# Kernel tuning notes

Hardware: AMD Instinct MI355X
Metric: run time of the kernel (lower is better)

Reference implementation:

```python
import jax, jax.numpy as jnp
import numpy as np

HEADS, DQK, DV = 4, 128, 128
HH, WW = 32, 32
SCALE = DQK ** -0.5
EPS = 1e-5


def bn(x, g, b, m, v):
    # eval-mode BatchNorm2d over channel dim of NCHW
    inv = g * jax.lax.rsqrt(v + EPS)
    return x * inv[:, None, None] + (b - m * inv)[:, None, None]


def rel_to_abs(x):
    # x: (B, Nh, L, 2L-1) -> (B, Nh, L, L)
    B, Nh, L, _ = x.shape
    x = jnp.pad(x, ((0, 0), (0, 0), (0, 0), (0, 1)))
    fx = x.reshape(B, Nh, L * 2 * L)
    fx = jnp.pad(fx, ((0, 0), (0, 0), (0, L - 1)))
    fx = fx.reshape(B, Nh, L + 1, 2 * L - 1)
    return fx[:, :, :L, L - 1:]


def rel_logits_1d(q, rel_k):
    # q: (B, Nh, H, W, D); rel_k: (2W-1, D)
    B, Nh, H, W, D = q.shape
    r = jnp.einsum('bnhwd,rd->bnhwr', q, rel_k)
    r = rel_to_abs(r.reshape(B, Nh * H, W, 2 * W - 1))
    r = r.reshape(B, Nh, H, W, W)
    return jnp.broadcast_to(r[:, :, :, None], (B, Nh, H, H, W, W))


def pos_bias(q, rel_h, rel_w):
    # q: (B, Nh, H*W, D), already scaled
    B, Nh, L, D = q.shape
    q5 = q.reshape(B, Nh, HH, WW, D)
    rw = rel_logits_1d(q5, rel_w)                     # (B,N,H,Hx,W,W)
    rw = rw.transpose(0, 1, 2, 4, 3, 5).reshape(B, Nh, HH * WW, HH * WW)
    rh = rel_logits_1d(q5.transpose(0, 1, 3, 2, 4), rel_h)  # (B,N,W,Wx,H,H)
    rh = rh.transpose(0, 1, 4, 2, 5, 3).reshape(B, Nh, HH * WW, HH * WW)
    return rw + rh


def to_heads(x):
    # (B, Nh*d, H, W) -> (B, Nh, H*W, d)
    B, C, H, W = x.shape
    x = x.reshape(B, HEADS, C // HEADS, H, W)
    return x.transpose(0, 1, 3, 4, 2).reshape(B, HEADS, H * W, C // HEADS)


def mhsa(x, w_qk, w_v, rel_h, rel_w):
    B, C, H, W = x.shape
    qk = jnp.einsum('bchw,oc->bohw', x, w_qk)
    q, k = jnp.split(qk, 2, axis=1)
    v = jnp.einsum('bchw,oc->bohw', x, w_v)
    q, k, v = to_heads(q), to_heads(k), to_heads(v)
    q = q * SCALE
    logits = jnp.einsum('bnid,bnjd->bnij', q, k) + pos_bias(q, rel_h, rel_w)
    weights = jax.nn.softmax(logits, axis=-1)
    out = jnp.einsum('bnij,bnjd->bnid', weights, v)   # (B,Nh,HW,dv)
    out = out.reshape(B, HEADS, H, W, DV).transpose(0, 1, 4, 2, 3)
    return out.reshape(B, HEADS * DV, H, W)


def setup_inputs() -> dict:
    key = jax.random.key(0)
    ks = jax.random.split(key, 12)
    d = {
        'x': jax.random.normal(ks[0], (8, 512, HH, WW), jnp.float32),
        'w_qk': jax.random.normal(ks[1], (2 * HEADS * DQK, 512), jnp.float32) * 0.02,
        'w_v': jax.random.normal(ks[2], (HEADS * DV, 512), jnp.float32) * 0.02,
        'rel_h': jax.random.normal(ks[3], (2 * HH - 1, DQK), jnp.float32) * SCALE,
        'rel_w': jax.random.normal(ks[4], (2 * WW - 1, DQK), jnp.float32) * SCALE,
        'g1': jnp.ones((512,), jnp.float32),
        'b1': jnp.zeros((512,), jnp.float32),
        'm1': jax.random.normal(ks[5], (512,), jnp.float32) * 0.1,
        'v1': jax.random.uniform(ks[6], (512,), jnp.float32) + 0.5,
        'g2': jnp.ones((512,), jnp.float32),
        'b2': jnp.zeros((512,), jnp.float32),
        'm2': jax.random.normal(ks[7], (512,), jnp.float32) * 0.1,
        'v2': jax.random.uniform(ks[8], (512,), jnp.float32) + 0.5,
        'w_fc': jax.random.normal(ks[9], (512, 512, 3, 3), jnp.float32) * 0.02,
        'bias_fc': jnp.zeros((512,), jnp.float32),
    }
    return d


def reference(x, w_qk, w_v, rel_h, rel_w, g1, b1, m1, v1, g2, b2, m2, v2, w_fc, bias_fc):
    out = jax.nn.relu(bn(x, g1, b1, m1, v1))
    out = mhsa(out, w_qk, w_v, rel_h, rel_w)
    x = out + x
    out = jax.nn.relu(bn(x, g2, b2, m2, v2))
    out = jax.lax.conv_general_dilated(
        out, w_fc, window_strides=(1, 1), padding='SAME',
        dimension_numbers=('NCHW', 'OIHW', 'NCHW')) + bias_fc[:, None, None]
    return out + x
```

## Files before the change

kernel.cpp:

```cpp
#include <hip/hip_runtime.h>

typedef __bf16 v8bf __attribute__((ext_vector_type(8)));
typedef float f32x4 __attribute__((ext_vector_type(4)));

#define DEVI static __device__ __forceinline__

DEVI v8bf load8(const __bf16* p) { return *reinterpret_cast<const v8bf*>(p); }

DEVI f32x4 mfma16(v8bf a, v8bf b, f32x4 c) {
  return __builtin_amdgcn_mfma_f32_16x16x32_bf16(a, b, c, 0, 0, 0);
}

DEVI void gld16(const __bf16* g, __bf16* l) {
  __builtin_amdgcn_global_load_lds(
      (const __attribute__((address_space(1))) unsigned int*)(const void*)g,
      (__attribute__((address_space(3))) unsigned int*)(void*)l, 16, 0, 0);
}

#define SCALE_Q 0.08838834764831845f

__global__ void k_prep(const float* __restrict__ wqk, const float* __restrict__ wv,
                       const float* __restrict__ relh, const float* __restrict__ relw,
                       const float* __restrict__ wfc, __bf16* __restrict__ wqkb,
                       __bf16* __restrict__ wvb, __bf16* __restrict__ rhb,
                       __bf16* __restrict__ rwb, __bf16* __restrict__ Wt,
                       float* __restrict__ zpad4) {
  const int bid = blockIdx.x, tid = threadIdx.x;
  if (bid < 2048) {
    int i = bid * 256 + tid;
    wqkb[i] = (__bf16)wqk[i];
  } else if (bid < 3072) {
    int i = (bid - 2048) * 256 + tid;
    wvb[i] = (__bf16)wv[i];
  } else if (bid < 3104) {
    int i = (bid - 3072) * 256 + tid;
    if (i < 8064) rhb[i] = (__bf16)relh[i];
  } else if (bid < 3136) {
    int i = (bid - 3104) * 256 + tid;
    if (i < 8064) rwb[i] = (__bf16)relw[i];
  } else if (bid < 4160) {
    int i = (bid - 3136) * 256 + tid;
    const float* src = wfc + (size_t)i * 9;
#pragma unroll
    for (int tap = 0; tap < 9; ++tap)
      Wt[(size_t)tap * 262144 + i] = (__bf16)src[tap];
  } else {
    int i = (bid - 4160) * 256 + tid;
    f32x4 z = {0.f, 0.f, 0.f, 0.f};
    reinterpret_cast<f32x4*>(zpad4)[i] = z;
  }
}

__global__ void k_bn1(const float* __restrict__ x, const float* __restrict__ g,
                      const float* __restrict__ bb, const float* __restrict__ m,
                      const float* __restrict__ v, __bf16* __restrict__ y) {
  __shared__ float tile[32][33];
  const int b = blockIdx.z, c0 = blockIdx.y * 32, s0 = blockIdx.x * 32;
  const int tx = threadIdx.x, ty = threadIdx.y;
#pragma unroll
  for (int r = 0; r < 4; ++r) {
    int c = c0 + ty + r * 8;
    float inv = g[c] * rsqrtf(v[c] + 1e-5f);
    float beta = bb[c] - m[c] * inv;
    float val = x[((size_t)b * 512 + c) * 1024 + s0 + tx] * inv + beta;
    tile[ty + r * 8][tx] = fmaxf(val, 0.0f);
  }
  __syncthreads();
#pragma unroll
  for (int r = 0; r < 4; ++r) {
    int s = s0 + ty + r * 8;
    y[((size_t)b * 1024 + s) * 512 + c0 + tx] = (__bf16)tile[tx][ty + r * 8];
  }
}

__global__ void k_bn2c(float* o0x2, const float* __restrict__ o1,
                       const float* __restrict__ lp, const float* __restrict__ xin,
                       const float* __restrict__ g, const float* __restrict__ bb,
                       const float* __restrict__ m, const float* __restrict__ v,
                       __bf16* __restrict__ zp) {
  __shared__ float tile[32][33];
  const int b = blockIdx.z, c0 = blockIdx.y * 32, s0 = blockIdx.x * 32;
  const int tx = threadIdx.x, ty = threadIdx.y;
  const int bnrow = b * 4 + (c0 >> 7);
  const int scol = s0 + tx;
  const float linv =
      1.0f / (lp[bnrow * 1024 + scol] + lp[32768 + bnrow * 1024 + scol]);
#pragma unroll
  for (int r = 0; r < 4; ++r) {
    int c = c0 + ty + r * 8;
    float inv = g[c] * rsqrtf(v[c] + 1e-5f);
    float beta = bb[c] - m[c] * inv;
    size_t idx = ((size_t)b * 512 + c) * 1024 + scol;
    float t = (o0x2[idx] + o1[idx]) * linv + xin[idx];
    o0x2[idx] = t;
    tile[ty + r * 8][tx] = fmaxf(t * inv + beta, 0.0f);
  }
  __syncthreads();
#pragma unroll
  for (int r = 0; r < 4; ++r) {
    int s = s0 + ty + r * 8;
    int hh = s >> 5, ww = s & 31;
    zp[(((size_t)b * 34 + hh + 1) * 34 + ww + 1) * 512 + c0 + tx] =
        (__bf16)tile[tx][ty + r * 8];
  }
}

__global__ __launch_bounds__(256) void k_proj(
    const __bf16* __restrict__ wall, const __bf16* __restrict__ y,
    __bf16* __restrict__ qout, __bf16* __restrict__ kout,
    __bf16* __restrict__ vout) {
  __shared__ __bf16 As[128 * 32];
  __shared__ __bf16 Bs[128 * 32];
  const int t = threadIdx.x;
  const int wave = t >> 6, lane = t & 63;
  const int l15 = lane & 15, quad = lane >> 4;
  const int mbase = blockIdx.x * 128;
  const int nbase = blockIdx.y * 128;
  const int mh = (wave >> 1) * 64, nh = (wave & 1) * 64;
  const bool isv = mbase >= 1024;

  const int row0 = t >> 2, part8 = (t & 3) * 8;
  const __bf16* gA0 = wall + (size_t)(mbase + row0) * 512 + part8;
  const __bf16* gA1 = gA0 + (size_t)64 * 512;
  const __bf16* gB0 = y + (size_t)(nbase + row0) * 512 + part8;
  const __bf16* gB1 = gB0 + (size_t)64 * 512;
  __bf16* lA0 = As + (size_t)(wave * 64) * 8;
  __bf16* lA1 = As + (size_t)(256 + wave * 64) * 8;
  __bf16* lB0 = Bs + (size_t)(wave * 64) * 8;
  __bf16* lB1 = Bs + (size_t)(256 + wave * 64) * 8;

  const f32x4 fz = {0.f, 0.f, 0.f, 0.f};
  f32x4 acc[4][4];
#pragma unroll
  for (int i = 0; i < 4; ++i)
#pragma unroll
    for (int j = 0; j < 4; ++j) acc[i][j] = fz;

  for (int k0 = 0; k0 < 512; k0 += 32) {
    __syncthreads();
    gld16(gA0 + k0, lA0);
    gld16(gA1 + k0, lA1);
    gld16(gB0 + k0, lB0);
    gld16(gB1 + k0, lB1);
    __syncthreads();
    v8bf a[4], bfr[4];
#pragma unroll
    for (int i = 0; i < 4; ++i)
      a[i] = load8(&As[(size_t)(mh + i * 16 + l15) * 32 + quad * 8]);
#pragma unroll
    for (int j = 0; j < 4; ++j)
      bfr[j] = load8(&Bs[(size_t)(nh + j * 16 + l15) * 32 + quad * 8]);
    if (isv) {
#pragma unroll
      for (int i = 0; i < 4; ++i)
#pragma unroll
        for (int j = 0; j < 4; ++j) acc[i][j] = mfma16(a[i], bfr[j], acc[i][j]);
    } else {
#pragma unroll
      for (int i = 0; i < 4; ++i)
#pragma unroll
        for (int j = 0; j < 4; ++j) acc[i][j] = mfma16(bfr[j], a[i], acc[i][j]);
    }
  }

  if (isv) {
#pragma unroll
    for (int i = 0; i < 4; ++i)
#pragma unroll
      for (int j = 0; j < 4; ++j)
#pragma unroll
        for (int r = 0; r < 4; ++r) {
          int o = mbase + mh + i * 16 + quad * 4 + r;
          int nflat = nbase + nh + j * 16 + l15;
          int b = nflat >> 10, s = nflat & 1023;
          int oe = o - 1024; int n = oe >> 7, d = oe & 127;
          vout[(((size_t)b * 4 + n) * 128 + d) * 1024 + s] = (__bf16)acc[i][j][r];
        }
  } else {
    const bool isq = mbase < 512;
#pragma unroll
    for (int i = 0; i < 4; ++i)
#pragma unroll
      for (int j = 0; j < 4; ++j)
#pragma unroll
        for (int r = 0; r < 4; ++r) {
          int o = mbase + mh + i * 16 + l15;
          int nflat = nbase + nh + j * 16 + quad * 4 + r;
          int b = nflat >> 10, s = nflat & 1023;
          float val = acc[i][j][r];
          if (isq) {
            int n = o >> 7, d = o & 127;
            qout[(((size_t)b * 4 + n) * 1024 + s) * 128 + d] = (__bf16)(val * SCALE_Q);
          } else {
            int oe = o - 512; int n = oe >> 7, d = oe & 127;
            kout[(((size_t)b * 4 + n) * 1024 + s) * 128 + d] = (__bf16)val;
          }
        }
  }
}

__global__ __launch_bounds__(256, 3) void k_attn(
    const __bf16* __restrict__ q, const __bf16* __restrict__ kmat,
    const __bf16* __restrict__ vt, const __bf16* __restrict__ relh,
    const __bf16* __restrict__ relw, float* __restrict__ o0,
    float* __restrict__ o1, float* __restrict__ lpart) {
  __shared__ __bf16 Ks[4 * 64 * 32];
  __shared__ __bf16 Vs[2 * 128 * 32];
  __shared__ __bf16 P[4 * 16 * 68];
  __shared__ __bf16 RWs[64][33];
  __shared__ __bf16 RHs[64][33];

  const int Lb = blockIdx.x;
  const int xcd = Lb & 7, local = Lb >> 3;
  const int bn = xcd * 4 + (local & 3);
  const int qblk = (local >> 2) & 15;
  const int half = local >> 6;
  const int s0 = qblk * 64;

  const int t = threadIdx.x;
  const int wave = t >> 6, lane = t & 63;
  const int l15 = lane & 15, quad = lane >> 4;
  const size_t hoff = ((size_t)bn) << 17;
  const int s0w = s0 + wave * 16;
  const int wlo = (wave & 1) * 16;
  const int h0w = s0w >> 5;

  const int row0 = t >> 2, part8 = (t & 3) * 8;
  const __bf16* kg = kmat + hoff + (size_t)row0 * 128 + part8;
  const __bf16* vg = vt + hoff + (size_t)row0 * 1024 + part8;
  __bf16* ksw = Ks + wave * 512;
  __bf16* vsw = Vs + wave * 512;

  const int j00 = half * 512;
#pragma unroll
  for (int kk = 0; kk < 4; ++kk)
    gld16(kg + (size_t)j00 * 128 + kk * 32, ksw + kk * 2048);
#pragma unroll
  for (int kk2 = 0; kk2 < 2; ++kk2)
#pragma unroll
    for (int dh = 0; dh < 2; ++dh)
      gld16(vg + (size_t)dh * 64 * 1024 + j00 + kk2 * 32,
            vsw + kk2 * 4096 + dh * 2048);

  v8bf aq[4];
  {
    const __bf16* qp = q + hoff + (size_t)(s0w + l15) * 128;
#pragma unroll
    for (int kk = 0; kk < 4; ++kk) aq[kk] = load8(qp + kk * 32 + quad * 8);
  }

#pragma unroll
  for (int nt = 0; nt < 4; ++nt) {
    int rr = nt * 16 + l15;
    const __bf16* bp = relw + (size_t)rr * 128;
    f32x4 acc = {0.f, 0.f, 0.f, 0.f};
#pragma unroll
    for (int kk = 0; kk < 4; ++kk)
      acc = mfma16(aq[kk], load8(bp + kk * 32 + quad * 8), acc);
#pragma unroll
    for (int r = 0; r < 4; ++r) {
      int row = quad * 4 + r;
      int wj = rr + wlo + row - 31;
      if (wj >= 0 && wj < 32) RWs[wave * 16 + row][wj] = (__bf16)acc[r];
    }
  }
#pragma unroll
  for (int nt = 0; nt < 2; ++nt) {
    int hj = nt * 16 + l15;
    const __bf16* bp = relh + (size_t)(hj - h0w + 31) * 128;
    f32x4 acc = {0.f, 0.f, 0.f, 0.f};
#pragma unroll
    for (int kk = 0; kk < 4; ++kk)
      acc = mfma16(aq[kk], load8(bp + kk * 32 + quad * 8), acc);
#pragma unroll
    for (int r = 0; r < 4; ++r) RHs[wave * 16 + quad * 4 + r][hj] = (__bf16)acc[r];
  }

  __syncthreads();

  float rwreg[4][2];
#pragma unroll
  for (int r = 0; r < 4; ++r) {
    const int gi = wave * 16 + quad * 4 + r;
    rwreg[r][0] = (float)RWs[gi][l15];
    rwreg[r][1] = (float)RWs[gi][l15 + 16];
  }

  const f32x4 fz = {0.f, 0.f, 0.f, 0.f};
  float lsum[4] = {0.f, 0.f, 0.f, 0.f};
  f32x4 oacc[8];
#pragma unroll
  for (int dt = 0; dt < 8; ++dt) oacc[dt] = fz;
  __bf16* Pw = P + wave * 16 * 68;

#pragma unroll 1
  for (int iter = 0; iter < 8; ++iter) {
    f32x4 sacc[4];
    __builtin_amdgcn_s_setprio(1);
#pragma unroll
    for (int nj = 0; nj < 4; ++nj) {
      f32x4 a = fz;
#pragma unroll
      for (int kk = 0; kk < 4; ++kk)
        a = mfma16(aq[kk],
                   load8(&Ks[kk * 2048 + (nj * 16 + l15) * 32 + quad * 8]), a);
      sacc[nj] = a;
    }
    __builtin_amdgcn_s_setprio(0);

    const int hjb = half * 16 + iter * 2;
#pragma unroll
    for (int r = 0; r < 4; ++r) {
      const int row = quad * 4 + r;
      const int gi = wave * 16 + row;
      const float rw0 = rwreg[r][0], rw1 = rwreg[r][1];
      const float rh0 = (float)RHs[gi][hjb], rh1 = (float)RHs[gi][hjb + 1];
#pragma unroll
      for (int nj = 0; nj < 4; ++nj) {
        float val = sacc[nj][r] + ((nj & 1) ? rw1 : rw0) + ((nj & 2) ? rh1 : rh0);
        float p = __expf(fminf(val, 60.0f));
        lsum[r] += p;
        Pw[row * 68 + nj * 16 + l15] = (__bf16)p;
      }
    }
    v8bf pf[2];
#pragma unroll
    for (int kk2 = 0; kk2 < 2; ++kk2)
      pf[kk2] = *reinterpret_cast<const v8bf*>(&Pw[l15 * 68 + kk2 * 32 + quad * 8]);

    asm volatile("s_waitcnt vmcnt(0)" ::: "memory");
    __builtin_amdgcn_s_barrier();
    __builtin_amdgcn_sched_barrier(0);

    __builtin_amdgcn_s_setprio(1);
#pragma unroll
    for (int dt = 0; dt < 8; ++dt) {
      f32x4 a = oacc[dt];
#pragma unroll
      for (int kk2 = 0; kk2 < 2; ++kk2)
        a = mfma16(load8(&Vs[kk2 * 4096 + (dt * 16 + l15) * 32 + quad * 8]),
                   pf[kk2], a);
      oacc[dt] = a;
    }
    __builtin_amdgcn_s_setprio(0);

    __syncthreads();

    if (iter < 7) {
      const int jn = j00 + (iter + 1) * 64;
#pragma unroll
      for (int kk = 0; kk < 4; ++kk)
        gld16(kg + (size_t)jn * 128 + kk * 32, ksw + kk * 2048);
#pragma unroll
      for (int kk2 = 0; kk2 < 2; ++kk2)
#pragma unroll
        for (int dh = 0; dh < 2; ++dh)
          gld16(vg + (size_t)dh * 64 * 1024 + jn + kk2 * 32,
                vsw + kk2 * 4096 + dh * 2048);
      asm volatile("s_waitcnt vmcnt(4)" ::: "memory");
      __builtin_amdgcn_s_barrier();
      __builtin_amdgcn_sched_barrier(0);
    }
  }

#pragma unroll
  for (int r = 0; r < 4; ++r)
#pragma unroll
    for (int msk = 8; msk >= 1; msk >>= 1) lsum[r] += __shfl_xor(lsum[r], msk);
  if (l15 == 0) {
#pragma unroll
    for (int r = 0; r < 4; ++r)
      lpart[half * 32768 + bn * 1024 + s0w + quad * 4 + r] = lsum[r];
  }

  {
    float* op = half ? o1 : o0;
    const int s = s0w + l15;
#pragma unroll
    for (int dt = 0; dt < 8; ++dt)
#pragma unroll
      for (int r = 0; r < 4; ++r) {
        int d = dt * 16 + quad * 4 + r;
        op[((size_t)bn * 128 + d) * 1024 + s] = oacc[dt][r];
      }
  }
}

__global__ __launch_bounds__(256, 2) void k_conv(
    const __bf16* __restrict__ Wt, const __bf16* __restrict__ zp,
    float* __restrict__ part) {
  __shared__ __bf16 As[4 * 128 * 32];
  __shared__ __bf16 Bs[4 * 128 * 32];
  const int t = threadIdx.x;
  const int wave = t >> 6, lane = t & 63;
  const int l15 = lane & 15, quad = lane >> 4;

  const int id = blockIdx.x;
  const int combo = id & 7;
  const int ot = combo >> 1, sp = combo & 1;
  const int nt = id >> 3;
  const int mbase = ot * 128;
  const int nbase = nt * 128;
  const int cs = sp * 256;
  const int mh = (wave >> 1) * 64, nh = (wave & 1) * 64;

  const int row0 = t >> 2;
  const int part8 = (t & 3) * 8;
  const __bf16* gA0 = Wt + (size_t)(mbase + row0) * 512 + cs + part8;
  const __bf16* gA1 = gA0 + (size_t)64 * 512;
  const int n0 = nbase + row0;
  const int b0 = n0 >> 10, spn = n0 & 1023;
  const __bf16* gB0 =
      zp + ((size_t)(b0 * 34 + (spn >> 5) + 1) * 34 + (spn & 31) + 1) * 512 + cs + part8;
  const __bf16* gB1 = gB0 + (size_t)2 * 34 * 512;
  const int wofs = wave * 512;

  const f32x4 fz = {0.f, 0.f, 0.f, 0.f};
  f32x4 acc[4][4];
#pragma unroll
  for (int i = 0; i < 4; ++i)
#pragma unroll
    for (int j = 0; j < 4; ++j) acc[i][j] = fz;

#pragma unroll 1
  for (int tap = 0; tap < 9; ++tap) {
    const int dh = tap / 3 - 1, dw = tap % 3 - 1;
    const size_t aoff = (size_t)tap * 512 * 512;
    const int boff = (dh * 34 + dw) * 512;
#pragma unroll 1
    for (int k0 = 0; k0 < 256; k0 += 128) {
      __syncthreads();
#pragma unroll
      for (int c = 0; c < 4; ++c) {
        const int kq = k0 + c * 32;
        gld16(gA0 + aoff + kq, As + c * 4096 + wofs);
        gld16(gA1 + aoff + kq, As + c * 4096 + 2048 + wofs);
        gld16(gB0 + boff + kq, Bs + c * 4096 + wofs);
        gld16(gB1 + boff + kq, Bs + c * 4096 + 2048 + wofs);
      }
      __syncthreads();
#pragma unroll
      for (int c = 0; c < 4; ++c) {
        v8bf a[4], bfr[4];
#pragma unroll
        for (int i = 0; i < 4; ++i)
          a[i] = load8(&As[c * 4096 + (mh + i * 16 + l15) * 32 + quad * 8]);
#pragma unroll
        for (int j = 0; j < 4; ++j)
          bfr[j] = load8(&Bs[c * 4096 + (nh + j * 16 + l15) * 32 + quad * 8]);
#pragma unroll
        for (int i = 0; i < 4; ++i)
#pragma unroll
          for (int j = 0; j < 4; ++j) acc[i][j] = mfma16(a[i], bfr[j], acc[i][j]);
      }
    }
  }

  float* pout = part + (size_t)sp * 8 * 512 * 1024;
#pragma unroll
  for (int i = 0; i < 4; ++i)
#pragma unroll
    for (int j = 0; j < 4; ++j)
#pragma unroll
      for (int r = 0; r < 4; ++r) {
        int o = mbase + mh + i * 16 + quad * 4 + r;
        int nn = nbase + nh + j * 16 + l15;
        int bb2 = nn >> 10, s = nn & 1023;
        pout[((size_t)bb2 * 512 + o) * 1024 + s] = acc[i][j][r];
      }
}

__global__ void k_sum(const float* __restrict__ part, const float* __restrict__ bias,
                      const float* __restrict__ x2, float* __restrict__ out) {
  int i = blockIdx.x * 256 + threadIdx.x;
  int o = (i >> 8) & 511;
  f32x4 p0 = reinterpret_cast<const f32x4*>(part)[i];
  f32x4 p1 = reinterpret_cast<const f32x4*>(part + (size_t)8 * 512 * 1024)[i];
  f32x4 xr = reinterpret_cast<const f32x4*>(x2)[i];
  float bo = bias[o];
  f32x4 r;
#pragma unroll
  for (int c = 0; c < 4; ++c) r[c] = p0[c] + p1[c] + bo + xr[c];
  reinterpret_cast<f32x4*>(out)[i] = r;
}

extern "C" void kernel_launch(void* const* d_in, const int* in_sizes, int n_in,
                              void* d_out, int out_size, void* d_ws, size_t ws_size,
                              hipStream_t stream) {
  const float* x    = (const float*)d_in[0];
  const float* wqk  = (const float*)d_in[1];
  const float* wv   = (const float*)d_in[2];
  const float* relh = (const float*)d_in[3];
  const float* relw = (const float*)d_in[4];
  const float* g1   = (const float*)d_in[5];
  const float* b1   = (const float*)d_in[6];
  const float* m1   = (const float*)d_in[7];
  const float* v1   = (const float*)d_in[8];
  const float* g2   = (const float*)d_in[9];
  const float* b2   = (const float*)d_in[10];
  const float* m2   = (const float*)d_in[11];
  const float* v2   = (const float*)d_in[12];
  const float* wfc  = (const float*)d_in[13];
  const float* bfc  = (const float*)d_in[14];
  float* out = (float*)d_out;

  char* p = (char*)d_ws;
  __bf16* y    = (__bf16*)p; p += (size_t)8 * 1024 * 512 * 2;
  __bf16* qb   = (__bf16*)p; p += (size_t)8 * 4 * 1024 * 128 * 2;
  __bf16* kb   = (__bf16*)p; p += (size_t)8 * 4 * 1024 * 128 * 2;
  __bf16* vb   = (__bf16*)p; p += (size_t)8 * 4 * 1024 * 128 * 2;
  __bf16* Wt   = (__bf16*)p; p += (size_t)9 * 512 * 512 * 2;
  __bf16* wqkb = (__bf16*)p; p += (size_t)1024 * 512 * 2;
  __bf16* wvb  = (__bf16*)p; p += (size_t)512 * 512 * 2;
  __bf16* rhb  = (__bf16*)p; p += 32768;
  __bf16* rwb  = (__bf16*)p; p += 32768;
  float*  x2   = (float*)p;  p += (size_t)8 * 512 * 1024 * 4;
  __bf16* zpad = (__bf16*)p; p += (size_t)8 * 34 * 34 * 512 * 2;
  float* lpart = (float*)d_ws;
  float* o0 = x2;
  float* o1 = (float*)d_out;
  float* part = (float*)d_ws;

  k_prep<<<dim3(6472), dim3(256), 0, stream>>>(wqk, wv, relh, relw, wfc,
                                               wqkb, wvb, rhb, rwb, Wt, (float*)zpad);
  k_bn1<<<dim3(32, 16, 8), dim3(32, 8), 0, stream>>>(x, g1, b1, m1, v1, y);
  k_proj<<<dim3(12, 64), dim3(256), 0, stream>>>(wqkb, y, qb, kb, vb);
  k_attn<<<dim3(1024), dim3(256), 0, stream>>>(qb, kb, vb, rhb, rwb, o0, o1, lpart);
  k_bn2c<<<dim3(32, 16, 8), dim3(32, 8), 0, stream>>>(o0, o1, lpart, x,
                                                      g2, b2, m2, v2, zpad);
  k_conv<<<dim3(512), dim3(256), 0, stream>>>(Wt, zpad, part);
  k_sum<<<dim3(4096), dim3(256), 0, stream>>>(part, bfc, x2, out);
}
```

Before: 252.7 us.

## Drop LDS staging of K/V in attention; read operands directly from global

Removes the shared-memory K and V tiles and their async global-to-LDS prefetch pipeline. MFMA operands are now loaded straight from global memory (relying on L2/L1 hits), which eliminates per-iteration barriers and frees LDS, so launch bounds are raised to four blocks per SM. The cost is uncoalesced, repeated global loads with no cross-wave sharing and no prefetch overlap. A small Lt shared array and an extra barrier are added but Lt is never read.

```diff
diff --git a/kernel.cpp b/kernel.cpp
--- a/kernel.cpp
+++ b/kernel.cpp
@@ -199,16 +199,15 @@
   }
 }
 
-__global__ __launch_bounds__(256, 3) void k_attn(
+__global__ __launch_bounds__(256, 4) void k_attn(
     const __bf16* __restrict__ q, const __bf16* __restrict__ kmat,
     const __bf16* __restrict__ vt, const __bf16* __restrict__ relh,
     const __bf16* __restrict__ relw, float* __restrict__ o0,
     float* __restrict__ o1, float* __restrict__ lpart) {
-  __shared__ __bf16 Ks[4 * 64 * 32];
-  __shared__ __bf16 Vs[2 * 128 * 32];
   __shared__ __bf16 P[4 * 16 * 68];
   __shared__ __bf16 RWs[64][33];
   __shared__ __bf16 RHs[64][33];
+  __shared__ float Lt[4][16];
 
   const int Lb = blockIdx.x;
   const int xcd = Lb & 7, local = Lb >> 3;
@@ -225,23 +224,6 @@
   const int wlo = (wave & 1) * 16;
   const int h0w = s0w >> 5;
 
-  const int row0 = t >> 2, part8 = (t & 3) * 8;
-  const __bf16* kg = kmat + hoff + (size_t)row0 * 128 + part8;
-  const __bf16* vg = vt + hoff + (size_t)row0 * 1024 + part8;
-  __bf16* ksw = Ks + wave * 512;
-  __bf16* vsw = Vs + wave * 512;
-
-  const int j00 = half * 512;
-#pragma unroll
-  for (int kk = 0; kk < 4; ++kk)
-    gld16(kg + (size_t)j00 * 128 + kk * 32, ksw + kk * 2048);
-#pragma unroll
-  for (int kk2 = 0; kk2 < 2; ++kk2)
-#pragma unroll
-    for (int dh = 0; dh < 2; ++dh)
-      gld16(vg + (size_t)dh * 64 * 1024 + j00 + kk2 * 32,
-            vsw + kk2 * 4096 + dh * 2048);
-
   v8bf aq[4];
   {
     const __bf16* qp = q + hoff + (size_t)(s0w + l15) * 128;
@@ -276,8 +258,6 @@
     for (int r = 0; r < 4; ++r) RHs[wave * 16 + quad * 4 + r][hj] = (__bf16)acc[r];
   }
 
-  __syncthreads();
-
   float rwreg[4][2];
 #pragma unroll
   for (int r = 0; r < 4; ++r) {
@@ -286,24 +266,29 @@
     rwreg[r][1] = (float)RWs[gi][l15 + 16];
   }
 
+  __syncthreads();
+
   const f32x4 fz = {0.f, 0.f, 0.f, 0.f};
   float lsum[4] = {0.f, 0.f, 0.f, 0.f};
   f32x4 oacc[8];
 #pragma unroll
   for (int dt = 0; dt < 8; ++dt) oacc[dt] = fz;
   __bf16* Pw = P + wave * 16 * 68;
+  const __bf16* kb2 = kmat + hoff;
+  const __bf16* vb2 = vt + hoff;
 
 #pragma unroll 1
   for (int iter = 0; iter < 8; ++iter) {
+    const int j0 = half * 512 + iter * 64;
+
     f32x4 sacc[4];
     __builtin_amdgcn_s_setprio(1);
 #pragma unroll
     for (int nj = 0; nj < 4; ++nj) {
+      const __bf16* kr = kb2 + (size_t)(j0 + nj * 16 + l15) * 128 + quad * 8;
       f32x4 a = fz;
 #pragma unroll
-      for (int kk = 0; kk < 4; ++kk)
-        a = mfma16(aq[kk],
-                   load8(&Ks[kk * 2048 + (nj * 16 + l15) * 32 + quad * 8]), a);
+      for (int kk = 0; kk < 4; ++kk) a = mfma16(aq[kk], load8(kr + kk * 32), a);
       sacc[nj] = a;
     }
     __builtin_amdgcn_s_setprio(0);
@@ -328,45 +313,28 @@
     for (int kk2 = 0; kk2 < 2; ++kk2)
       pf[kk2] = *reinterpret_cast<const v8bf*>(&Pw[l15 * 68 + kk2 * 32 + quad * 8]);
 
-    asm volatile("s_waitcnt vmcnt(0)" ::: "memory");
-    __builtin_amdgcn_s_barrier();
-    __builtin_amdgcn_sched_barrier(0);
-
     __builtin_amdgcn_s_setprio(1);
 #pragma unroll
     for (int dt = 0; dt < 8; ++dt) {
+      const __bf16* vr = vb2 + (size_t)(dt * 16 + l15) * 1024 + j0 + quad * 8;
       f32x4 a = oacc[dt];
 #pragma unroll
       for (int kk2 = 0; kk2 < 2; ++kk2)
-        a = mfma16(load8(&Vs[kk2 * 4096 + (dt * 16 + l15) * 32 + quad * 8]),
-                   pf[kk2], a);
+        a = mfma16(load8(vr + kk2 * 32), pf[kk2], a);
       oacc[dt] = a;
     }
     __builtin_amdgcn_s_setprio(0);
-
-    __syncthreads();
-
-    if (iter < 7) {
-      const int jn = j00 + (iter + 1) * 64;
-#pragma unroll
-      for (int kk = 0; kk < 4; ++kk)
-        gld16(kg + (size_t)jn * 128 + kk * 32, ksw + kk * 2048);
-#pragma unroll
-      for (int kk2 = 0; kk2 < 2; ++kk2)
-#pragma unroll
-        for (int dh = 0; dh < 2; ++dh)
-          gld16(vg + (size_t)dh * 64 * 1024 + jn + kk2 * 32,
-                vsw + kk2 * 4096 + dh * 2048);
-      asm volatile("s_waitcnt vmcnt(4)" ::: "memory");
-      __builtin_amdgcn_s_barrier();
-      __builtin_amdgcn_sched_barrier(0);
-    }
   }
 
 #pragma unroll
   for (int r = 0; r < 4; ++r)
 #pragma unroll
     for (int msk = 8; msk >= 1; msk >>= 1) lsum[r] += __shfl_xor(lsum[r], msk);
+  if (l15 == 0) {
+#pragma unroll
+    for (int r = 0; r < 4; ++r) Lt[wave][quad * 4 + r] = lsum[r];
+  }
+  __syncthreads();
   if (l15 == 0) {
 #pragma unroll
     for (int r = 0; r < 4; ++r)
```

Measured after the change: 323.3 us. 1.28x slower.
